# Kernel tuning notes

Hardware: AMD Instinct MI355X
Metric: run time of the kernel (lower is better)

Reference implementation:

```python
import jax, jax.numpy as jnp
import numpy as np

L = 2        # n_layers
F = 128      # in_features == out_features (GRUCell + highway constraint)
O = 128
N = 1024     # nodes
B = 8        # batch
D = 3        # edge directions (weight.size(0))


def setup_inputs() -> dict:
    key = jax.random.key(0)
    ks = jax.random.split(key, 10)
    s = 1.0 / np.sqrt(F)
    u = lambda k, shp: jax.random.uniform(k, shp, jnp.float32, minval=-s, maxval=s)
    return {
        "inputs": jax.random.normal(ks[0], (N, B, F), jnp.float32),
        "adj": jax.random.uniform(ks[1], (D, B, N, N), jnp.float32),
        "W": u(ks[2], (L, D, F, O)),            # GCN weight per layer/direction
        "Bc": u(ks[3], (L, D, O)),              # GCN bias
        "Wh": u(ks[4], (L, F, O)),              # highway weight
        "Bh": u(ks[5], (L, O)),                 # highway bias
        "Wih": u(ks[6], (L, 3 * O, O)),         # GRUCell input weights
        "Whh": u(ks[7], (L, 3 * O, O)),         # GRUCell hidden weights
        "bih": u(ks[8], (L, 3 * O)),
        "bhh": u(ks[9], (L, 3 * O)),
    }


def _gru(x, h, wih, whh, bih, bhh):
    # torch.nn.GRUCell semantics; x,h: [..., O]
    gi = x @ wih.T + bih
    gh = h @ whh.T + bhh
    i_r, i_z, i_n = jnp.split(gi, 3, axis=-1)
    h_r, h_z, h_n = jnp.split(gh, 3, axis=-1)
    r = jax.nn.sigmoid(i_r + h_r)
    z = jax.nn.sigmoid(i_z + h_z)
    n = jnp.tanh(i_n + r * h_n)
    return (1.0 - z) * n + z * h


def reference(inputs, adj, W, Bc, Wh, Bh, Wih, Whh, bih, bhh):
    x = inputs  # [N, B, F]; dropout layers are identity at eval
    for l in range(L):
        # support per direction: [D, B, N, O]
        support = jnp.einsum('nbf,dfo->dbno', x, W[l]) + Bc[l][:, None, None, :]
        # adjacency-weighted aggregation: adj[d,b] @ support[d,b]
        agg = jnp.einsum('dbmn,dbno->dbmo', adj, support)
        # GRU update with hidden = current features, per direction, summed over d
        h = jnp.broadcast_to(jnp.transpose(x, (1, 0, 2))[None], agg.shape)
        hnew = _gru(agg, h, Wih[l], Whh[l], bih[l], bhh[l])
        out = jnp.transpose(jnp.sum(hnew, axis=0), (1, 0, 2))  # [N, B, O]
        out = jax.nn.relu(out)  # activation='relu'
        # highway gate (highway='relu')
        t = jax.nn.relu(jnp.einsum('nbf,fo->nbo', x, Wh[l]) + Bh[l])
        x = out * t + x * (1.0 - t)
    return x
```

## Files before the change

kernel.cpp:

```cpp
#include <hip/hip_runtime.h>
#include <math.h>

#define N_NODES 1024
#define BATCH   8
#define FEAT    128
#define NDIR    3
#define NB      (N_NODES*BATCH)
#define G3      384

typedef __bf16 bf16_t;
using bf16x8 = __attribute__((ext_vector_type(8))) __bf16;
using bf16x4 = __attribute__((ext_vector_type(4))) __bf16;
using f32x4  = __attribute__((ext_vector_type(4))) float;

#define GLOAD_LDS16(g, l) \
    __builtin_amdgcn_global_load_lds((const __attribute__((address_space(1))) void*)(g), \
                                     (__attribute__((address_space(3))) void*)(l), 16, 0, 0)

template<int R>
__device__ __forceinline__ void stage_swz(const bf16_t* __restrict__ src, int stride,
                                          int k0, bf16_t* lds, int w, int lane)
{
    #pragma unroll
    for (int q = 0; q < R/32; ++q) {
        int rbase = w*(R/4) + q*8;
        int row = rbase + (lane >> 3);
        int seg = (lane & 7) ^ (row & 7);
        GLOAD_LDS16(src + (size_t)row*stride + k0 + seg*8,
                    (char*)lds + (size_t)rbase*128);
    }
}

__device__ __forceinline__ void stageA_issue(const float* __restrict__ src, int k0,
                                             float4 (&r)[4], int w, int lane)
{
    #pragma unroll
    for (int q = 0; q < 2; ++q) {
        int row = w*16 + q*8 + (lane >> 3);
        int seg = (lane & 7) ^ (row & 7);
        const float* g = src + (size_t)row*1024 + k0 + seg*8;
        r[q*2+0] = *reinterpret_cast<const float4*>(g);
        r[q*2+1] = *reinterpret_cast<const float4*>(g + 4);
    }
}

__device__ __forceinline__ void stageA_commit(const float4 (&r)[4], bf16_t* lds,
                                              int w, int lane)
{
    #pragma unroll
    for (int q = 0; q < 2; ++q) {
        int row = w*16 + q*8 + (lane >> 3);
        int s   = lane & 7;
        float4 v0 = r[q*2+0], v1 = r[q*2+1];
        bf16x8 pk;
        pk[0]=(bf16_t)(v0.x-0.5f); pk[1]=(bf16_t)(v0.y-0.5f);
        pk[2]=(bf16_t)(v0.z-0.5f); pk[3]=(bf16_t)(v0.w-0.5f);
        pk[4]=(bf16_t)(v1.x-0.5f); pk[5]=(bf16_t)(v1.y-0.5f);
        pk[6]=(bf16_t)(v1.z-0.5f); pk[7]=(bf16_t)(v1.w-0.5f);
        *reinterpret_cast<bf16x8*>(&lds[row*64 + s*8]) = pk;
    }
}

template<int MI, int NJ>
__device__ __forceinline__ void mfma_swz(const bf16_t* As, const bf16_t* Bs,
                                         f32x4 (&acc)[MI][NJ], int wr, int wc, int lane)
{
    #pragma unroll
    for (int ks = 0; ks < 64; ks += 32) {
        int bslot = ks/8 + (lane >> 4);
        int sx = bslot ^ (lane & 7);
        bf16x8 af[MI], bfv[NJ];
        #pragma unroll
        for (int i = 0; i < MI; ++i) {
            int row = wr*MI*16 + i*16 + (lane & 15);
            af[i] = *reinterpret_cast<const bf16x8*>(&As[row*64 + sx*8]);
        }
        #pragma unroll
        for (int j = 0; j < NJ; ++j) {
            int row = wc*NJ*16 + j*16 + (lane & 15);
            bfv[j] = *reinterpret_cast<const bf16x8*>(&Bs[row*64 + sx*8]);
        }
        #pragma unroll
        for (int i = 0; i < MI; ++i) {
            #pragma unroll
            for (int j = 0; j < NJ; ++j)
                acc[i][j] = __builtin_amdgcn_mfma_f32_16x16x32_bf16(af[i], bfv[j], acc[i][j], 0, 0, 0);
        }
    }
}

__device__ __forceinline__ float fast_sigmoid(float x)
{
    float t = __builtin_amdgcn_exp2f(-1.442695041f * x);
    return __builtin_amdgcn_rcpf(1.0f + t);
}
__device__ __forceinline__ float fast_tanh(float x)
{
    float ax = fabsf(x);
    float t = __builtin_amdgcn_exp2f(-2.885390082f * ax);
    float r = (1.0f - t) * __builtin_amdgcn_rcpf(1.0f + t);
    return copysignf(r, x);
}

__global__ __launch_bounds__(128) void k_wprep(
    const float* __restrict__ W, const float* __restrict__ Wh,
    const float* __restrict__ Whh, const float* __restrict__ Wih,
    bf16_t* __restrict__ wsup,
    bf16_t* __restrict__ wihc)
{
    int m = blockIdx.x, l = blockIdx.y, k = threadIdx.x;
    float w;
    bf16_t* dst;
    bool patB = false;
    if (m < 384) {
        int d = m >> 7, o = m & 127;
        w = W[((size_t)(l*3 + d)*128 + k)*128 + o];
        dst = wsup + ((size_t)l*896 + m)*384;
    } else if (m < 512) {
        int o = m - 384;
        w = Wh[((size_t)l*128 + k)*128 + o];
        dst = wsup + ((size_t)l*896 + m)*384;
    } else if (m < 896) {
        int c = m - 512;
        w = Whh[((size_t)l*384 + c)*128 + k];
        dst = wsup + ((size_t)l*896 + m)*384;
    } else {
        int c = m - 896;
        w = Wih[((size_t)l*384 + c)*128 + k];
        dst = wihc + ((size_t)l*384 + c)*384;
        patB = true;
    }
    bf16_t hi = (bf16_t)w;
    bf16_t lo = (bf16_t)(w - (float)hi);
    if (patB) { dst[k] = hi; dst[128 + k] = hi; dst[256 + k] = lo; }
    else      { dst[k] = hi; dst[128 + k] = lo; dst[256 + k] = hi; }
}

__global__ __launch_bounds__(256) void k_xcat(
    const float* __restrict__ X, bf16_t* __restrict__ xcat,
    float* __restrict__ colsum2)
{
    int idx = blockIdx.x * 256 + threadIdx.x;
    if (idx < 2*3072) colsum2[idx] = 0.0f;
    int k = idx & 127, r = idx >> 7;
    int n = r >> 3, b = r & 7;
    float v = X[idx];
    bf16_t hi = (bf16_t)v;
    bf16_t lo = (bf16_t)(v - (float)hi);
    bf16_t* dst = xcat + ((size_t)(b*1024 + n))*384 + k;
    dst[0] = hi; dst[128] = hi; dst[256] = lo;
}

__global__ __launch_bounds__(256, 2) void k_sup2(
    const bf16_t* __restrict__ Wcat,
    const bf16_t* __restrict__ xcat,
    const float* __restrict__ Bcl,
    const float* __restrict__ Bhl,
    const float* __restrict__ bhhl,
    bf16_t* __restrict__ supt,
    float* __restrict__ tbuf,
    bf16_t* __restrict__ ghb,
    float* __restrict__ colsum)
{
    __shared__ bf16_t As[2][128*64];
    __shared__ bf16_t Bs[2][128*64];
    const int t = threadIdx.x, lane = t & 63, w = t >> 6;
    const int wr = w >> 1, wc = w & 1;
    const int n0 = blockIdx.x * 128;
    const int m0 = blockIdx.y * 128;
    const int b  = blockIdx.z;
    const bf16_t* Arow = Wcat + (size_t)m0 * 384;
    const bf16_t* Brow = xcat + ((size_t)b * 1024 + n0) * 384;

    f32x4 acc[4][4] = {};
    stage_swz<128>(Arow, 384, 0, As[0], w, lane);
    stage_swz<128>(Brow, 384, 0, Bs[0], w, lane);
    __syncthreads();
    #pragma unroll
    for (int kt = 0; kt < 6; ++kt) {
        if (kt + 1 < 6) {
            stage_swz<128>(Arow, 384, (kt+1)*64, As[(kt+1)&1], w, lane);
            stage_swz<128>(Brow, 384, (kt+1)*64, Bs[(kt+1)&1], w, lane);
        }
        mfma_swz<4,4>(As[kt&1], Bs[kt&1], acc, wr, wc, lane);
        __syncthreads();
    }
    #pragma unroll
    for (int i = 0; i < 4; ++i) {
        int mb = m0 + wr*64 + i*16 + ((lane >> 4) * 4);
        if (mb < 384) {
            #pragma unroll
            for (int rg = 0; rg < 4; ++rg) {
                int m = mb + rg;
                int d = m >> 7, o = m & 127;
                float bv = Bcl[d*128 + o];
                float psum = 0.0f;
                #pragma unroll
                for (int j = 0; j < 4; ++j) {
                    int n = n0 + wc*64 + j*16 + (lane & 15);
                    bf16_t sv = (bf16_t)(acc[i][j][rg] + bv);
                    supt[((size_t)((d*8 + b)*128 + o))*1024 + n] = sv;
                    psum += (float)sv;
                }
                psum += __shfl_xor(psum, 1, 64);
                psum += __shfl_xor(psum, 2, 64);
                psum += __shfl_xor(psum, 4, 64);
                psum += __shfl_xor(psum, 8, 64);
                if ((lane & 15) == 0)
                    atomicAdd(&colsum[(d*8 + b)*128 + o], psum);
            }
        } else if (mb < 512) {
            #pragma unroll
            for (int j = 0; j < 4; ++j) {
                int n = n0 + wc*64 + j*16 + (lane & 15);
                #pragma unroll
                for (int rg = 0; rg < 4; ++rg) {
                    int o = mb + rg - 384;
                    tbuf[((size_t)(b*128 + o))*1024 + n] =
                        fmaxf(acc[i][j][rg] + Bhl[o], 0.0f);
                }
            }
        } else {
            #pragma unroll
            for (int j = 0; j < 4; ++j) {
                int n = n0 + wc*64 + j*16 + (lane & 15);
                int c = mb - 512;
                bf16x4 pk;
                #pragma unroll
                for (int rg = 0; rg < 4; ++rg)
                    pk[rg] = (bf16_t)(acc[i][j][rg] + bhhl[c + rg]);
                *reinterpret_cast<bf16x4*>(&ghb[((size_t)(b*1024 + n))*384 + c]) = pk;
            }
        }
    }
}

__device__ __forceinline__ int aggls_off(int row, int k)
{
    return row*256 + (((k >> 3) ^ (row & 15)) << 3) + (k & 7);
}

__global__ __launch_bounds__(256, 2) void k_aggi(
    const float* __restrict__ adjf,
    const bf16_t* __restrict__ supt,
    const float* __restrict__ colsum,
    const bf16_t* __restrict__ wihcL,
    const float* __restrict__ biasL,
    bf16_t* __restrict__ girz,
    float* __restrict__ gin)
{
    __shared__ char pool[49152];
    __shared__ bf16_t aggls[64*256];
    bf16_t* As  = (bf16_t*)pool;
    bf16_t* Bs  = (bf16_t*)(pool + 16384);
    bf16_t* BsG = (bf16_t*)pool;

    const int t = threadIdx.x, lane = t & 63, w = t >> 6;
    const int wr = w >> 1, wc = w & 1;
    const int m0 = blockIdx.x * 64;
    const int z  = blockIdx.y;
    const float*  Af   = adjf + (size_t)z * 1024 * 1024 + (size_t)m0 * 1024;
    const bf16_t* Brow = supt + (size_t)z * 128 * 1024;

    f32x4 acc[2][4] = {};
    float4 ra[4];
    stageA_issue(Af, 0, ra, w, lane);
    stage_swz<128>(Brow, 1024, 0, Bs, w, lane);
    stageA_commit(ra, As, w, lane);
    __syncthreads();
    #pragma unroll
    for (int kt = 0; kt < 16; ++kt) {
        if (kt + 1 < 16) {
            stageA_issue(Af, (kt+1)*64, ra, w, lane);
            stage_swz<128>(Brow, 1024, (kt+1)*64, Bs + ((kt+1)&1)*8192, w, lane);
        }
        mfma_swz<2,4>(As + (kt&1)*4096, Bs + (kt&1)*8192, acc, wr, wc, lane);
        if (kt + 1 < 16)
            stageA_commit(ra, As + ((kt+1)&1)*4096, w, lane);
        __syncthreads();
    }

    stage_swz<128>(wihcL, 384, 0, BsG, w, lane);

    #pragma unroll
    for (int i = 0; i < 2; ++i) {
        #pragma unroll
        for (int rg = 0; rg < 4; ++rg) {
            int row = wr*32 + i*16 + ((lane >> 4) * 4) + rg;
            #pragma unroll
            for (int j = 0; j < 4; ++j) {
                int o = wc*64 + j*16 + (lane & 15);
                float v = acc[i][j][rg] + 0.5f * colsum[z*128 + o];
                bf16_t hi = (bf16_t)v;
                bf16_t lo = (bf16_t)(v - (float)hi);
                aggls[aggls_off(row, o)]       = hi;
                aggls[aggls_off(row, 128 + o)] = lo;
            }
        }
    }
    __syncthreads();

    #pragma unroll
    for (int cc = 0; cc < 3; ++cc) {
        f32x4 a2[2][4] = {};
        #pragma unroll
        for (int kt = 0; kt < 6; ++kt) {
            int it = cc*6 + kt;
            if (it + 1 < 18) {
                int nc = (it+1)/6, nk = (it+1)%6;
                stage_swz<128>(wihcL + (size_t)nc*128*384, 384, nk*64,
                               BsG + ((it+1)&1)*8192, w, lane);
            }
            const bf16_t* Bcur = BsG + (it&1)*8192;
            int akk = (kt < 4 ? kt : kt - 4) * 64;
            #pragma unroll
            for (int ks = 0; ks < 64; ks += 32) {
                bf16x8 af[2], bfv[4];
                #pragma unroll
                for (int i = 0; i < 2; ++i) {
                    int row = wr*32 + i*16 + (lane & 15);
                    int ss = ((akk + ks)/8 + (lane >> 4)) ^ (lane & 15);
                    af[i] = *reinterpret_cast<const bf16x8*>(&aggls[row*256 + ss*8]);
                }
                #pragma unroll
                for (int j = 0; j < 4; ++j) {
                    int row = wc*64 + j*16 + (lane & 15);
                    int sx = (ks/8 + (lane >> 4)) ^ (lane & 7);
                    bfv[j] = *reinterpret_cast<const bf16x8*>(&Bcur[row*64 + sx*8]);
                }
                #pragma unroll
                for (int i = 0; i < 2; ++i) {
                    #pragma unroll
                    for (int j = 0; j < 4; ++j)
                        a2[i][j] = __builtin_amdgcn_mfma_f32_16x16x32_bf16(af[i], bfv[j], a2[i][j], 0, 0, 0);
                }
            }
            __syncthreads();
        }
        #pragma unroll
        for (int j = 0; j < 4; ++j) {
            int c = cc*128 + wc*64 + j*16 + (lane & 15);
            float bv = biasL[c];
            #pragma unroll
            for (int i = 0; i < 2; ++i) {
                #pragma unroll
                for (int rg = 0; rg < 4; ++rg) {
                    int rloc = wr*32 + i*16 + ((lane >> 4) * 4) + rg;
                    size_t m = (size_t)z*1024 + m0 + rloc;
                    float v = a2[i][j][rg] + bv;
                    if (c < 256) girz[m*256 + c] = (bf16_t)v;
                    else         gin[m*128 + (c - 256)] = v;
                }
            }
        }
    }
}

__global__ __launch_bounds__(256) void k_gates(
    const bf16_t* __restrict__ girz, const float* __restrict__ gin,
    const bf16_t* __restrict__ ghb,
    bf16_t* xcat,
    const float* __restrict__ tbuf,
    float* __restrict__ Xout, int write_xcat)
{
    __shared__ float ts[128*17];
    const int b = blockIdx.y, n0 = blockIdx.x * 16;
    const int tid = threadIdx.x;
    {
        int o = tid >> 1, nh = (tid & 1) * 8;
        const float* src = tbuf + ((size_t)(b*128 + o))*1024 + n0 + nh;
        float4 v0 = *reinterpret_cast<const float4*>(src);
        float4 v1 = *reinterpret_cast<const float4*>(src + 4);
        float* dst = &ts[o*17 + nh];
        dst[0]=v0.x; dst[1]=v0.y; dst[2]=v0.z; dst[3]=v0.w;
        dst[4]=v1.x; dst[5]=v1.y; dst[6]=v1.z; dst[7]=v1.w;
    }
    __syncthreads();
    #pragma unroll
    for (int p = 0; p < 8; ++p) {
        int e = p*256 + tid;
        int nn = e >> 7, o = e & 127;
        int n = n0 + nn;
        size_t rb = (size_t)(b*1024 + n);
        bf16_t* xr = xcat + rb*384;
        float h = (float)xr[o] + (float)xr[256 + o];
        const bf16_t* ghr = ghb + rb*G3;
        float g_r = (float)ghr[o], g_z = (float)ghr[128+o], g_n = (float)ghr[256+o];
        float acc = 0.0f;
        #pragma unroll
        for (int d = 0; d < 3; ++d) {
            size_t rr = (size_t)((d*8 + b)*1024 + n);
            float i_r = (float)girz[rr*256 + o];
            float i_z = (float)girz[rr*256 + 128 + o];
            float i_n = gin[rr*128 + o];
            float rg = fast_sigmoid(i_r + g_r);
            float zg = fast_sigmoid(i_z + g_z);
            float ng = fast_tanh(i_n + rg * g_n);
            acc += (1.0f - zg) * ng + zg * h;
        }
        float outv = fmaxf(acc, 0.0f);
        float tg = ts[o*17 + nn];
        float res = outv * tg + h * (1.0f - tg);
        if (Xout) Xout[(size_t)(n*8 + b)*128 + o] = res;
        if (write_xcat) {
            bf16_t hi = (bf16_t)res;
            bf16_t lo = (bf16_t)(res - (float)hi);
            xr[o] = hi; xr[128 + o] = hi; xr[256 + o] = lo;
        }
    }
}

extern "C" void kernel_launch(void* const* d_in, const int* in_sizes, int n_in,
                              void* d_out, int out_size, void* d_ws, size_t ws_size,
                              hipStream_t stream) {
    const float* inputs = (const float*)d_in[0];
    const float* adj    = (const float*)d_in[1];
    const float* W      = (const float*)d_in[2];
    const float* Bc     = (const float*)d_in[3];
    const float* Wh     = (const float*)d_in[4];
    const float* Bh     = (const float*)d_in[5];
    const float* Wih    = (const float*)d_in[6];
    const float* Whh    = (const float*)d_in[7];
    const float* bih    = (const float*)d_in[8];
    const float* bhh    = (const float*)d_in[9];

    char* ws = (char*)d_ws;
    float*  tbuf   = (float*)ws;   ws += (size_t)8*128*1024*4;
    bf16_t* xcat   = (bf16_t*)ws;  ws += (size_t)8*1024*384*2;
    bf16_t* ghb    = (bf16_t*)ws;  ws += (size_t)NB*G3*2;
    bf16_t* supt   = (bf16_t*)ws;  ws += (size_t)24*128*1024*2;
    bf16_t* girz   = (bf16_t*)ws;  ws += (size_t)3*NB*256*2;
    float*  gin    = (float*)ws;   ws += (size_t)3*NB*128*4;
    float*  colsum2= (float*)ws;   ws += (size_t)2*24*128*4;
    bf16_t* wsup   = (bf16_t*)ws;  ws += (size_t)2*896*384*2;
    bf16_t* wihc   = (bf16_t*)ws;

    k_wprep<<<dim3(1280, 2), dim3(128), 0, stream>>>(W, Wh, Whh, Wih, wsup, wihc);
    k_xcat<<<dim3(4096), dim3(256), 0, stream>>>(inputs, xcat, colsum2);

    for (int l = 0; l < 2; ++l) {
        float* colsum = colsum2 + l*3072;
        k_sup2<<<dim3(8, 7, 8), dim3(256), 0, stream>>>(
            wsup + (size_t)l*896*384, xcat, Bc + l*3*128, Bh + l*128, bhh + l*G3,
            supt, tbuf, ghb, colsum);
        k_aggi<<<dim3(16, 24), dim3(256), 0, stream>>>(
            adj, supt, colsum, wihc + (size_t)l*384*384, bih + l*G3, girz, gin);
        k_gates<<<dim3(64, 8), dim3(256), 0, stream>>>(
            girz, gin, ghb, xcat, tbuf,
            (l == 1) ? (float*)d_out : (float*)nullptr, (l == 0) ? 1 : 0);
    }
}
```

Baseline: 289.9 us.

## Deepen the prefetch pipeline with manual vmcnt waits and raised MFMA priority

Both GEMM phases now prefetch further ahead and replace full __syncthreads with hand-placed s_waitcnt vmcnt and s_barrier. In the aggregation loop, A tiles use two register sets and B tiles are staged two iterations ahead, so more global loads are in flight during the MFMAs. The GRU-input GEMM cycles the pool memory as three weight buffers with a distance-two prefetch. MFMA sections run under s_setprio(1) to favour the compute waves. The hand-counted vmcnt values depend on how many loads each stage issues, so a wrong count would quietly read stale LDS data.

Result: no change. 285.2 us (-1.6%).

```diff
diff --git a/kernel.cpp b/kernel.cpp
--- a/kernel.cpp
+++ b/kernel.cpp
@@ -16,6 +16,11 @@
 #define GLOAD_LDS16(g, l) \
     __builtin_amdgcn_global_load_lds((const __attribute__((address_space(1))) void*)(g), \
                                      (__attribute__((address_space(3))) void*)(l), 16, 0, 0)
+
+#define WAITV0 asm volatile("s_waitcnt vmcnt(0)" ::: "memory")
+#define WAITV4 asm volatile("s_waitcnt vmcnt(4)" ::: "memory")
+#define BARRIER_LG asm volatile("s_waitcnt lgkmcnt(0)\n\ts_barrier" ::: "memory")
+#define BARRIER_PL asm volatile("s_barrier" ::: "memory")
 
 template<int R>
 __device__ __forceinline__ void stage_swz(const bf16_t* __restrict__ src, int stride,
@@ -263,25 +268,34 @@
     const bf16_t* Brow = supt + (size_t)z * 128 * 1024;
 
     f32x4 acc[2][4] = {};
-    float4 ra[4];
-    stageA_issue(Af, 0, ra, w, lane);
+    float4 ra[2][4];
+
     stage_swz<128>(Brow, 1024, 0, Bs, w, lane);
-    stageA_commit(ra, As, w, lane);
-    __syncthreads();
+    stageA_issue(Af, 0, ra[0], w, lane);
+    WAITV0;
+    stageA_commit(ra[0], As, w, lane);
+    stage_swz<128>(Brow, 1024, 64, Bs + 8192, w, lane);
+    stageA_issue(Af, 64, ra[1], w, lane);
+    stageA_issue(Af, 128, ra[0], w, lane);
+    BARRIER_LG;
+
     #pragma unroll
     for (int kt = 0; kt < 16; ++kt) {
-        if (kt + 1 < 16) {
-            stageA_issue(Af, (kt+1)*64, ra, w, lane);
-            stage_swz<128>(Brow, 1024, (kt+1)*64, Bs + ((kt+1)&1)*8192, w, lane);
-        }
+        __builtin_amdgcn_s_setprio(1);
         mfma_swz<2,4>(As + (kt&1)*4096, Bs + (kt&1)*8192, acc, wr, wc, lane);
-        if (kt + 1 < 16)
-            stageA_commit(ra, As + ((kt+1)&1)*4096, w, lane);
-        __syncthreads();
+        __builtin_amdgcn_s_setprio(0);
+        if (kt <= 13)      { WAITV4; }
+        else if (kt == 14) { WAITV0; }
+        if (kt < 15)
+            stageA_commit(ra[(kt+1)&1], As + ((kt+1)&1)*4096, w, lane);
+        BARRIER_LG;
+        if (kt + 2 < 16)
+            stage_swz<128>(Brow, 1024, (kt+2)*64, Bs + (kt&1)*8192, w, lane);
+        if (kt + 3 < 16)
+            stageA_issue(Af, (kt+3)*64, ra[(kt+1)&1], w, lane);
     }
 
     stage_swz<128>(wihcL, 384, 0, BsG, w, lane);
-
     #pragma unroll
     for (int i = 0; i < 2; ++i) {
         #pragma unroll
@@ -298,21 +312,19 @@
             }
         }
     }
-    __syncthreads();
+    stage_swz<128>(wihcL, 384, 64, BsG + 8192, w, lane);
+    WAITV4;
+    BARRIER_LG;
 
     #pragma unroll
     for (int cc = 0; cc < 3; ++cc) {
         f32x4 a2[2][4] = {};
         #pragma unroll
-        for (int kt = 0; kt < 6; ++kt) {
-            int it = cc*6 + kt;
-            if (it + 1 < 18) {
-                int nc = (it+1)/6, nk = (it+1)%6;
-                stage_swz<128>(wihcL + (size_t)nc*128*384, 384, nk*64,
-                               BsG + ((it+1)&1)*8192, w, lane);
-            }
-            const bf16_t* Bcur = BsG + (it&1)*8192;
-            int akk = (kt < 4 ? kt : kt - 4) * 64;
+        for (int kt6 = 0; kt6 < 6; ++kt6) {
+            const int it = cc*6 + kt6;
+            const bf16_t* Bcur = BsG + (it % 3)*8192;
+            int akk = (kt6 < 4 ? kt6 : kt6 - 4) * 64;
+            __builtin_amdgcn_s_setprio(1);
             #pragma unroll
             for (int ks = 0; ks < 64; ks += 32) {
                 bf16x8 af[2], bfv[4];
@@ -335,7 +347,15 @@
                         a2[i][j] = __builtin_amdgcn_mfma_f32_16x16x32_bf16(af[i], bfv[j], a2[i][j], 0, 0, 0);
                 }
             }
-            __syncthreads();
+            __builtin_amdgcn_s_setprio(0);
+            if (it + 2 < 18) {
+                const int ni = it + 2;
+                stage_swz<128>(wihcL + (size_t)(ni/6)*128*384, 384, (ni%6)*64,
+                               BsG + (ni % 3)*8192, w, lane);
+            }
+            if (it <= 15)      { WAITV4; }
+            else if (it == 16) { WAITV0; }
+            BARRIER_PL;
         }
         #pragma unroll
         for (int j = 0; j < 4; ++j) {
```
